# Optimization experiments

Hardware: AMD Instinct MI355X
Metric: run time of the kernel (lower is better)

## Reference

```python
import jax, jax.numpy as jnp
import numpy as np

N_NODES = 50000
N_EDGES = 800000
NFEAT = 512
NHID = 128
NCLASS = 40


def setup_inputs() -> dict:
    key = jax.random.key(0)
    ks = jax.random.split(key, 12)
    s = lambda fan_in: 1.0 / np.sqrt(fan_in)
    return {
        "x": jax.random.normal(ks[0], (N_NODES, NFEAT), dtype=jnp.float32),
        "edge_src": jax.random.randint(ks[1], (N_EDGES,), 0, N_NODES, dtype=jnp.int32),
        "edge_dst": jax.random.randint(ks[2], (N_EDGES,), 0, N_NODES, dtype=jnp.int32),
        "edge_val": jax.random.uniform(ks[3], (N_EDGES,), dtype=jnp.float32) * 0.1,
        # GraphConvolution 1: nfeat -> nhid
        "W1": jax.random.uniform(ks[4], (NFEAT, NHID), jnp.float32, -s(NFEAT), s(NFEAT)),
        "b1": jnp.zeros((NHID,), jnp.float32),
        # res1 Linear: nfeat -> nhid (stored as [in, out])
        "Wr1": jax.random.uniform(ks[5], (NFEAT, NHID), jnp.float32, -s(NFEAT), s(NFEAT)),
        "br1": jnp.zeros((NHID,), jnp.float32),
        # GraphConvolution 2: 2*nhid -> nclass
        "W2": jax.random.uniform(ks[6], (2 * NHID, NCLASS), jnp.float32, -s(2 * NHID), s(2 * NHID)),
        "b2": jnp.zeros((NCLASS,), jnp.float32),
        # res2 Linear: 2*nhid -> nclass
        "Wr2": jax.random.uniform(ks[7], (2 * NHID, NCLASS), jnp.float32, -s(2 * NHID), s(2 * NHID)),
        "br2": jnp.zeros((NCLASS,), jnp.float32),
    }


def _spmm(edge_src, edge_dst, edge_val, support):
    # adj @ support with adj in COO form: out[d] += val * support[s]
    msgs = edge_val[:, None] * support[edge_src]  # [E, F] irregular gather
    return jax.ops.segment_sum(msgs, edge_dst, num_segments=N_NODES)


def reference(x, edge_src, edge_dst, edge_val, W1, b1, Wr1, br1, W2, b2, Wr2, br2):
    # gc1(x, adj) = adj @ (x @ W1) + b1
    gc1 = _spmm(edge_src, edge_dst, edge_val, x @ W1) + b1
    h = jnp.concatenate([jax.nn.relu(gc1), x @ Wr1 + br1], axis=1)  # [N, 2*nhid]
    # dropout is identity in eval mode
    gc2 = _spmm(edge_src, edge_dst, edge_val, h @ W2) + b2
    h2 = gc2 + (h @ Wr2 + br2)
    return jax.nn.log_softmax(h2, axis=1)
```

## Files before the change

### kernel.cpp

```cpp
#include <hip/hip_runtime.h>
#include <stdint.h>

#define N_NODES 50000
#define N_EDGES 800000
#define NFEAT 512
#define NHID 128
#define NCLASS 40
#define NB 196

typedef __attribute__((ext_vector_type(8))) __bf16 bf16x8;
typedef __attribute__((ext_vector_type(4))) float f32x4;

__device__ __forceinline__ uint16_t f2b(float f) {
  uint32_t x = __float_as_uint(f);
  uint32_t r = (x + 0x7fffu + ((x >> 16) & 1u)) >> 16;
  return (uint16_t)r;
}
__device__ __forceinline__ float b2f(uint16_t u) {
  return __uint_as_float(((uint32_t)u) << 16);
}

__global__ void k_prep_w1(const float* __restrict__ W1, const float* __restrict__ Wr1,
                          uint16_t* __restrict__ WT) {
  int idx = blockIdx.x * 256 + threadIdx.x;
  if (idx >= 256 * 512) return;
  int n = idx >> 9, k = idx & 511;
  float v = (n < 128) ? W1[(size_t)k * 128 + n] : Wr1[(size_t)k * 128 + (n - 128)];
  WT[idx] = f2b(v);
}

__global__ void k_prep_w2(const float* __restrict__ W2, const float* __restrict__ Wr2,
                          uint16_t* __restrict__ WT) {
  int idx = blockIdx.x * 256 + threadIdx.x;
  if (idx >= 128 * 256) return;
  int n = idx >> 8, k = idx & 255;
  float v = 0.f;
  if (n < 40) v = W2[(size_t)k * 40 + n];
  else if (n < 80) v = Wr2[(size_t)k * 40 + (n - 40)];
  WT[idx] = f2b(v);
}

__global__ void k_hist(const int* __restrict__ dst, int* __restrict__ counts) {
  int e = blockIdx.x * 256 + threadIdx.x;
  if (e < N_EDGES) atomicAdd(&counts[dst[e]], 1);
}

__global__ void k_blocksum(const int* __restrict__ counts, int* __restrict__ blocksums) {
  __shared__ int red[256];
  int t = threadIdx.x, idx = blockIdx.x * 256 + t;
  red[t] = (idx < N_NODES) ? counts[idx] : 0;
  __syncthreads();
  for (int o = 128; o; o >>= 1) {
    if (t < o) red[t] += red[t + o];
    __syncthreads();
  }
  if (t == 0) blocksums[blockIdx.x] = red[0];
}

__global__ void k_scan2(const int* __restrict__ counts, const int* __restrict__ blocksums,
                        int* __restrict__ offs) {
  __shared__ int red[256];
  __shared__ int sc[256];
  int b = blockIdx.x, t = threadIdx.x;
  red[t] = (t < b && t < NB) ? blocksums[t] : 0;
  __syncthreads();
  for (int o = 128; o; o >>= 1) {
    if (t < o) red[t] += red[t + o];
    __syncthreads();
  }
  int prefix = red[0];
  int idx = b * 256 + t;
  int c = (idx < N_NODES) ? counts[idx] : 0;
  sc[t] = c;
  __syncthreads();
  for (int o = 1; o < 256; o <<= 1) {
    int v = (t >= o) ? sc[t - o] : 0;
    __syncthreads();
    sc[t] += v;
    __syncthreads();
  }
  if (idx <= N_NODES) offs[idx] = prefix + sc[t] - c;
}

__global__ void k_scatter(const int* __restrict__ src, const int* __restrict__ dst,
                          const float* __restrict__ val, const int* __restrict__ offs,
                          int* __restrict__ cursor, int2* __restrict__ es) {
  int e = blockIdx.x * 256 + threadIdx.x;
  if (e >= N_EDGES) return;
  int d = dst[e];
  int pos = offs[d] + atomicAdd(&cursor[d], 1);
  es[pos] = make_int2(src[e], __float_as_int(val[e]));
}

__global__ __launch_bounds__(512) void k_gemm1_fused(
    const float* __restrict__ x, const uint16_t* __restrict__ BT,
    uint16_t* __restrict__ S1b, uint16_t* __restrict__ h, const float* __restrict__ br1) {
  __shared__ uint16_t Al[128 * 72];
  __shared__ uint16_t Bl[256 * 64];
  const int tid = threadIdx.x;
  const int w = tid >> 6, lane = tid & 63;
  const int wm = w >> 2, wn = w & 3;
  const int m0 = blockIdx.x * 128;
  const int M = N_NODES;

  f32x4 acc[4][4];
#pragma unroll
  for (int t = 0; t < 4; t++)
#pragma unroll
    for (int u = 0; u < 4; u++) acc[t][u] = (f32x4)0.f;

  const int arow = tid >> 2;
  const int aslot = tid & 3;
  int ar = m0 + arow;
  if (ar >= M) ar = M - 1;
  const float* gxbase = x + (size_t)ar * NFEAT + aslot * 16;

  for (int kb = 0; kb < 8; ++kb) {
    __syncthreads();
    const int k0 = kb * 64;
    {
      const float4* gp = (const float4*)(gxbase + k0);
      float4 f0 = gp[0], f1 = gp[1], f2 = gp[2], f3 = gp[3];
      union { uint16_t u[8]; uint4 v; } o0, o1;
      o0.u[0] = f2b(f0.x); o0.u[1] = f2b(f0.y); o0.u[2] = f2b(f0.z); o0.u[3] = f2b(f0.w);
      o0.u[4] = f2b(f1.x); o0.u[5] = f2b(f1.y); o0.u[6] = f2b(f1.z); o0.u[7] = f2b(f1.w);
      o1.u[0] = f2b(f2.x); o1.u[1] = f2b(f2.y); o1.u[2] = f2b(f2.z); o1.u[3] = f2b(f2.w);
      o1.u[4] = f2b(f3.x); o1.u[5] = f2b(f3.y); o1.u[6] = f2b(f3.z); o1.u[7] = f2b(f3.w);
      *(uint4*)&Al[arow * 72 + aslot * 16] = o0.v;
      *(uint4*)&Al[arow * 72 + aslot * 16 + 8] = o1.v;
    }
#pragma unroll
    for (int i = 0; i < 4; i++) {
      int chunk = w * 4 + i;
      const uint16_t* gB = BT + (size_t)(chunk * 8 + (lane >> 3)) * NFEAT + k0 + (lane & 7) * 8;
      __builtin_amdgcn_global_load_lds(
          (const __attribute__((address_space(1))) void*)gB,
          (__attribute__((address_space(3))) void*)&Bl[chunk * 512], 16, 0, 0);
    }
    __syncthreads();
#pragma unroll
    for (int s = 0; s < 2; s++) {
      bf16x8 av[4], bv[4];
#pragma unroll
      for (int t = 0; t < 4; t++)
        av[t] = *(const bf16x8*)&Al[(wm * 64 + t * 16 + (lane & 15)) * 72 + s * 32 + (lane >> 4) * 8];
#pragma unroll
      for (int u = 0; u < 4; u++)
        bv[u] = *(const bf16x8*)&Bl[(wn * 64 + u * 16 + (lane & 15)) * 64 + s * 32 + (lane >> 4) * 8];
#pragma unroll
      for (int t = 0; t < 4; t++)
#pragma unroll
        for (int u = 0; u < 4; u++)
          acc[t][u] = __builtin_amdgcn_mfma_f32_16x16x32_bf16(av[t], bv[u], acc[t][u], 0, 0, 0);
    }
  }

  const int cl = lane & 15, rq = lane >> 4;
#pragma unroll
  for (int t = 0; t < 4; t++) {
#pragma unroll
    for (int u = 0; u < 4; u++) {
#pragma unroll
      for (int r = 0; r < 4; r++) {
        int m = m0 + wm * 64 + t * 16 + rq * 4 + r;
        int n = wn * 64 + u * 16 + cl;
        if (m >= M) continue;
        float v = acc[t][u][r];
        if (n < 128)
          S1b[(size_t)m * 128 + n] = f2b(v);
        else
          h[(size_t)m * 256 + n] = f2b(v + br1[n - 128]);
      }
    }
  }
}

__global__ __launch_bounds__(256, 2) void k_gemm2(
    const uint16_t* __restrict__ A, const uint16_t* __restrict__ BT, int M,
    uint16_t* __restrict__ S2b, float* __restrict__ oacc,
    const float* __restrict__ b2, const float* __restrict__ br2) {
  __shared__ uint16_t Al[128 * 64];
  __shared__ uint16_t Bl[128 * 64];
  const int tid = threadIdx.x;
  const int w = tid >> 6, lane = tid & 63;
  const int wm = w >> 1, wn = w & 1;
  const int m0 = blockIdx.x * 128;
  const int K = 256;

  f32x4 acc[4][4];
#pragma unroll
  for (int t = 0; t < 4; t++)
#pragma unroll
    for (int u = 0; u < 4; u++) acc[t][u] = (f32x4)0.f;

  const int lrow = lane >> 3;
  const int lcol = lane & 7;

  for (int kb = 0; kb < K / 64; ++kb) {
    __syncthreads();
    const int k0 = kb * 64;
#pragma unroll
    for (int i = 0; i < 4; i++) {
      int rr = (w * 4 + i) * 8 + lrow;
      int ra = m0 + rr;
      if (ra >= M) ra = M - 1;
      const uint16_t* gA = A + (size_t)ra * K + k0 + lcol * 8;
      __builtin_amdgcn_global_load_lds(
          (const __attribute__((address_space(1))) void*)gA,
          (__attribute__((address_space(3))) void*)&Al[(w * 4 + i) * 512], 16, 0, 0);
      const uint16_t* gB = BT + (size_t)rr * K + k0 + lcol * 8;
      __builtin_amdgcn_global_load_lds(
          (const __attribute__((address_space(1))) void*)gB,
          (__attribute__((address_space(3))) void*)&Bl[(w * 4 + i) * 512], 16, 0, 0);
    }
    __syncthreads();
#pragma unroll
    for (int s = 0; s < 2; s++) {
      bf16x8 av[4], bv[4];
#pragma unroll
      for (int t = 0; t < 4; t++)
        av[t] = *(const bf16x8*)&Al[(wm * 64 + t * 16 + (lane & 15)) * 64 + s * 32 + (lane >> 4) * 8];
#pragma unroll
      for (int u = 0; u < 4; u++)
        bv[u] = *(const bf16x8*)&Bl[(wn * 64 + u * 16 + (lane & 15)) * 64 + s * 32 + (lane >> 4) * 8];
#pragma unroll
      for (int t = 0; t < 4; t++)
#pragma unroll
        for (int u = 0; u < 4; u++)
          acc[t][u] = __builtin_amdgcn_mfma_f32_16x16x32_bf16(av[t], bv[u], acc[t][u], 0, 0, 0);
    }
  }

  const int cl = lane & 15, rq = lane >> 4;
#pragma unroll
  for (int t = 0; t < 4; t++) {
#pragma unroll
    for (int u = 0; u < 4; u++) {
#pragma unroll
      for (int r = 0; r < 4; r++) {
        int m = m0 + wm * 64 + t * 16 + rq * 4 + r;
        int n = wn * 64 + u * 16 + cl;
        if (m >= M) continue;
        float v = acc[t][u][r];
        if (n < 40) S2b[(size_t)m * 64 + n] = f2b(v);
        else if (n < 64) S2b[(size_t)m * 64 + n] = 0;
        if (n >= 40 && n < 80) oacc[(size_t)m * 64 + (n - 40)] = v + b2[n - 40] + br2[n - 40];
        else if (n >= 80 && n < 104) oacc[(size_t)m * 64 + (n - 40)] = 0.f;
      }
    }
  }
}

__global__ void k_spmm1_csr(const int* __restrict__ offs, const int2* __restrict__ es,
                            const uint16_t* __restrict__ S1b, const float* __restrict__ b1,
                            uint16_t* __restrict__ h) {
  int node = blockIdx.x * 4 + (threadIdx.x >> 6);
  if (node >= N_NODES) return;
  int lane = threadIdx.x & 63;
  int eg = lane >> 4;
  int fg = lane & 15;
  int beg = offs[node], end = offs[node + 1];
  float a[8];
#pragma unroll
  for (int j = 0; j < 8; j++) a[j] = 0.f;
  for (int p = beg; p < end; p += 4) {
    int pe = p + eg;
    bool ok = pe < end;
    int2 ev = es[ok ? pe : beg];
    float v = ok ? __int_as_float(ev.y) : 0.f;
    uint4 g = *(const uint4*)(S1b + (size_t)ev.x * 128 + fg * 8);
    a[0] += v * b2f((uint16_t)g.x); a[1] += v * b2f((uint16_t)(g.x >> 16));
    a[2] += v * b2f((uint16_t)g.y); a[3] += v * b2f((uint16_t)(g.y >> 16));
    a[4] += v * b2f((uint16_t)g.z); a[5] += v * b2f((uint16_t)(g.z >> 16));
    a[6] += v * b2f((uint16_t)g.w); a[7] += v * b2f((uint16_t)(g.w >> 16));
  }
#pragma unroll
  for (int j = 0; j < 8; j++) {
    a[j] += __shfl_xor(a[j], 16, 64);
    a[j] += __shfl_xor(a[j], 32, 64);
  }
  if (eg == 0) {
    const float4* bp = (const float4*)(b1 + fg * 8);
    float4 ba = bp[0], bb = bp[1];
    float r0 = a[0] + ba.x, r1 = a[1] + ba.y, r2 = a[2] + ba.z, r3 = a[3] + ba.w;
    float r4 = a[4] + bb.x, r5 = a[5] + bb.y, r6 = a[6] + bb.z, r7 = a[7] + bb.w;
    union { uint16_t u[8]; uint4 v; } o;
    o.u[0] = f2b(r0 > 0.f ? r0 : 0.f); o.u[1] = f2b(r1 > 0.f ? r1 : 0.f);
    o.u[2] = f2b(r2 > 0.f ? r2 : 0.f); o.u[3] = f2b(r3 > 0.f ? r3 : 0.f);
    o.u[4] = f2b(r4 > 0.f ? r4 : 0.f); o.u[5] = f2b(r5 > 0.f ? r5 : 0.f);
    o.u[6] = f2b(r6 > 0.f ? r6 : 0.f); o.u[7] = f2b(r7 > 0.f ? r7 : 0.f);
    *(uint4*)(h + (size_t)node * 256 + fg * 8) = o.v;
  }
}

__global__ void k_spmm2_lsm(const int* __restrict__ offs, const int2* __restrict__ es,
                            const uint16_t* __restrict__ S2b, const float* __restrict__ oacc,
                            float* __restrict__ out) {
  int node = blockIdx.x * 4 + (threadIdx.x >> 6);
  if (node >= N_NODES) return;
  int lane = threadIdx.x & 63;
  int eg = lane >> 3;
  int fg = lane & 7;
  int beg = offs[node], end = offs[node + 1];
  float a[8];
#pragma unroll
  for (int j = 0; j < 8; j++) a[j] = 0.f;
  for (int p = beg; p < end; p += 8) {
    int pe = p + eg;
    bool ok = pe < end;
    int2 ev = es[ok ? pe : beg];
    float v = ok ? __int_as_float(ev.y) : 0.f;
    uint4 g = *(const uint4*)(S2b + (size_t)ev.x * 64 + fg * 8);
    a[0] += v * b2f((uint16_t)g.x); a[1] += v * b2f((uint16_t)(g.x >> 16));
    a[2] += v * b2f((uint16_t)g.y); a[3] += v * b2f((uint16_t)(g.y >> 16));
    a[4] += v * b2f((uint16_t)g.z); a[5] += v * b2f((uint16_t)(g.z >> 16));
    a[6] += v * b2f((uint16_t)g.w); a[7] += v * b2f((uint16_t)(g.w >> 16));
  }
#pragma unroll
  for (int j = 0; j < 8; j++) {
    a[j] += __shfl_xor(a[j], 8, 64);
    a[j] += __shfl_xor(a[j], 16, 64);
    a[j] += __shfl_xor(a[j], 32, 64);
  }
  const float4* op = (const float4*)(oacc + (size_t)node * 64 + fg * 8);
  float4 o0 = op[0], o1 = op[1];
  float v0 = a[0] + o0.x, v1 = a[1] + o0.y, v2 = a[2] + o0.z, v3 = a[3] + o0.w;
  float v4 = a[4] + o1.x, v5 = a[5] + o1.y, v6 = a[6] + o1.z, v7 = a[7] + o1.w;
  bool valid = fg < 5;
  float m01 = v0 > v1 ? v0 : v1, m23 = v2 > v3 ? v2 : v3;
  float m45 = v4 > v5 ? v4 : v5, m67 = v6 > v7 ? v6 : v7;
  float ml = m01 > m23 ? m01 : m23;
  float mh = m45 > m67 ? m45 : m67;
  float mv = ml > mh ? ml : mh;
  mv = valid ? mv : -1e30f;
#pragma unroll
  for (int o = 1; o <= 4; o <<= 1) {
    float t = __shfl_xor(mv, o, 64);
    mv = mv > t ? mv : t;
  }
  float se = 0.f;
  if (valid)
    se = __expf(v0 - mv) + __expf(v1 - mv) + __expf(v2 - mv) + __expf(v3 - mv) +
         __expf(v4 - mv) + __expf(v5 - mv) + __expf(v6 - mv) + __expf(v7 - mv);
#pragma unroll
  for (int o = 1; o <= 4; o <<= 1) se += __shfl_xor(se, o, 64);
  if (eg == 0 && valid) {
    float ls = mv + __logf(se);
    float4 r0 = make_float4(v0 - ls, v1 - ls, v2 - ls, v3 - ls);
    float4 r1 = make_float4(v4 - ls, v5 - ls, v6 - ls, v7 - ls);
    float4* wp = (float4*)(out + (size_t)node * 40 + fg * 8);
    wp[0] = r0;
    wp[1] = r1;
  }
}

extern "C" void kernel_launch(void* const* d_in, const int* in_sizes, int n_in,
                              void* d_out, int out_size, void* d_ws, size_t ws_size,
                              hipStream_t stream) {
  const float* x = (const float*)d_in[0];
  const int* esrc = (const int*)d_in[1];
  const int* edst = (const int*)d_in[2];
  const float* eval = (const float*)d_in[3];
  const float* W1 = (const float*)d_in[4];
  const float* b1 = (const float*)d_in[5];
  const float* Wr1 = (const float*)d_in[6];
  const float* br1 = (const float*)d_in[7];
  const float* W2 = (const float*)d_in[8];
  const float* b2 = (const float*)d_in[9];
  const float* Wr2 = (const float*)d_in[10];
  const float* br2 = (const float*)d_in[11];
  float* out = (float*)d_out;

  char* ws = (char*)d_ws;
  uint16_t* S1b  = (uint16_t*)(ws);
  uint16_t* h    = (uint16_t*)(ws + 12800000);
  uint16_t* WT1  = (uint16_t*)(ws + 38400000);
  uint16_t* WT2  = (uint16_t*)(ws + 38662144);
  uint16_t* S2b  = (uint16_t*)(ws + 38727680);
  float*    oacc = (float*)(ws + 45127680);
  int*      counts = (int*)(ws + 57927680);
  int*      cursor = (int*)(ws + 58127680);
  int*      offs   = (int*)(ws + 58327680);
  int2*     es     = (int2*)(ws + 58527744);
  int*      blocksums = (int*)(ws + 64927744);

  hipMemsetAsync(counts, 0, 400000, stream);

  k_prep_w1<<<(256 * 512) / 256, 256, 0, stream>>>(W1, Wr1, WT1);
  k_prep_w2<<<(128 * 256) / 256, 256, 0, stream>>>(W2, Wr2, WT2);

  k_hist<<<(N_EDGES + 255) / 256, 256, 0, stream>>>(edst, counts);
  k_blocksum<<<NB, 256, 0, stream>>>(counts, blocksums);
  k_scan2<<<NB, 256, 0, stream>>>(counts, blocksums, offs);
  k_scatter<<<(N_EDGES + 255) / 256, 256, 0, stream>>>(esrc, edst, eval, offs, cursor, es);

  k_gemm1_fused<<<391, 512, 0, stream>>>(x, WT1, S1b, h, br1);

  k_spmm1_csr<<<(N_NODES + 3) / 4, 256, 0, stream>>>(offs, es, S1b, b1, h);

  k_gemm2<<<391, 256, 0, stream>>>(h, WT2, N_NODES, S2b, oacc, b2, br2);

  k_spmm2_lsm<<<(N_NODES + 3) / 4, 256, 0, stream>>>(offs, es, S2b, oacc, out);
}
```

Measured before the change: 364.7 us.

## Split x bf16 cast into separate kernel and tile GEMM1 over N

Adds a standalone kernel that casts x to bf16 in workspace, then rewrites GEMM1 to load both A and B tiles into LDS with direct global-to-LDS loads. GEMM1 now uses 256-thread blocks over a 2D grid (128x128 tiles) instead of 512-thread blocks covering all 256 output columns. The intent is to remove the in-loop fp32 load and convert work and raise occupancy. In exchange it adds an extra 100 MB of global read plus a 51 MB write for the bf16 copy, and x is read once per N tile.

```diff
diff --git a/kernel.cpp b/kernel.cpp
--- a/kernel.cpp
+++ b/kernel.cpp
@@ -18,6 +18,17 @@
 }
 __device__ __forceinline__ float b2f(uint16_t u) {
   return __uint_as_float(((uint32_t)u) << 16);
+}
+
+__global__ void k_cast_x(const float* __restrict__ x, uint16_t* __restrict__ xb, int n8) {
+  int i = blockIdx.x * blockDim.x + threadIdx.x;
+  if (i >= n8) return;
+  const float4* p = (const float4*)x + (size_t)i * 2;
+  float4 a = p[0], b = p[1];
+  union { uint16_t u[8]; uint4 v; } o;
+  o.u[0] = f2b(a.x); o.u[1] = f2b(a.y); o.u[2] = f2b(a.z); o.u[3] = f2b(a.w);
+  o.u[4] = f2b(b.x); o.u[5] = f2b(b.y); o.u[6] = f2b(b.z); o.u[7] = f2b(b.w);
+  ((uint4*)xb)[i] = o.v;
 }
 
 __global__ void k_prep_w1(const float* __restrict__ W1, const float* __restrict__ Wr1,
@@ -92,16 +103,17 @@
   es[pos] = make_int2(src[e], __float_as_int(val[e]));
 }
 
-__global__ __launch_bounds__(512) void k_gemm1_fused(
-    const float* __restrict__ x, const uint16_t* __restrict__ BT,
+__global__ __launch_bounds__(256, 2) void k_gemm1(
+    const uint16_t* __restrict__ A, const uint16_t* __restrict__ BT, int M,
     uint16_t* __restrict__ S1b, uint16_t* __restrict__ h, const float* __restrict__ br1) {
-  __shared__ uint16_t Al[128 * 72];
-  __shared__ uint16_t Bl[256 * 64];
+  __shared__ uint16_t Al[128 * 64];
+  __shared__ uint16_t Bl[128 * 64];
   const int tid = threadIdx.x;
   const int w = tid >> 6, lane = tid & 63;
-  const int wm = w >> 2, wn = w & 3;
+  const int wm = w >> 1, wn = w & 1;
   const int m0 = blockIdx.x * 128;
-  const int M = N_NODES;
+  const int n0 = blockIdx.y * 128;
+  const int K = NFEAT;
 
   f32x4 acc[4][4];
 #pragma unroll
@@ -109,33 +121,26 @@
 #pragma unroll
     for (int u = 0; u < 4; u++) acc[t][u] = (f32x4)0.f;
 
-  const int arow = tid >> 2;
-  const int aslot = tid & 3;
-  int ar = m0 + arow;
-  if (ar >= M) ar = M - 1;
-  const float* gxbase = x + (size_t)ar * NFEAT + aslot * 16;
-
-  for (int kb = 0; kb < 8; ++kb) {
+  const int lrow = lane >> 3;
+  const int lcol = lane & 7;
+
+  for (int kb = 0; kb < K / 64; ++kb) {
     __syncthreads();
     const int k0 = kb * 64;
-    {
-      const float4* gp = (const float4*)(gxbase + k0);
-      float4 f0 = gp[0], f1 = gp[1], f2 = gp[2], f3 = gp[3];
-      union { uint16_t u[8]; uint4 v; } o0, o1;
-      o0.u[0] = f2b(f0.x); o0.u[1] = f2b(f0.y); o0.u[2] = f2b(f0.z); o0.u[3] = f2b(f0.w);
-      o0.u[4] = f2b(f1.x); o0.u[5] = f2b(f1.y); o0.u[6] = f2b(f1.z); o0.u[7] = f2b(f1.w);
-      o1.u[0] = f2b(f2.x); o1.u[1] = f2b(f2.y); o1.u[2] = f2b(f2.z); o1.u[3] = f2b(f2.w);
-      o1.u[4] = f2b(f3.x); o1.u[5] = f2b(f3.y); o1.u[6] = f2b(f3.z); o1.u[7] = f2b(f3.w);
-      *(uint4*)&Al[arow * 72 + aslot * 16] = o0.v;
-      *(uint4*)&Al[arow * 72 + aslot * 16 + 8] = o1.v;
-    }
 #pragma unroll
     for (int i = 0; i < 4; i++) {
-      int chunk = w * 4 + i;
-      const uint16_t* gB = BT + (size_t)(chunk * 8 + (lane >> 3)) * NFEAT + k0 + (lane & 7) * 8;
+      int rr = (w * 4 + i) * 8 + lrow;
+      int ra = m0 + rr;
+      if (ra >= M) ra = M - 1;
+      const uint16_t* gA = A + (size_t)ra * K + k0 + lcol * 8;
+      __builtin_amdgcn_global_load_lds(
+          (const __attribute__((address_space(1))) void*)gA,
+          (__attribute__((address_space(3))) void*)&Al[(w * 4 + i) * 512], 16, 0, 0);
+      int rb = n0 + rr;
+      const uint16_t* gB = BT + (size_t)rb * K + k0 + lcol * 8;
       __builtin_amdgcn_global_load_lds(
           (const __attribute__((address_space(1))) void*)gB,
-          (__attribute__((address_space(3))) void*)&Bl[chunk * 512], 16, 0, 0);
+          (__attribute__((address_space(3))) void*)&Bl[(w * 4 + i) * 512], 16, 0, 0);
     }
     __syncthreads();
 #pragma unroll
@@ -143,7 +148,7 @@
       bf16x8 av[4], bv[4];
 #pragma unroll
       for (int t = 0; t < 4; t++)
-        av[t] = *(const bf16x8*)&Al[(wm * 64 + t * 16 + (lane & 15)) * 72 + s * 32 + (lane >> 4) * 8];
+        av[t] = *(const bf16x8*)&Al[(wm * 64 + t * 16 + (lane & 15)) * 64 + s * 32 + (lane >> 4) * 8];
 #pragma unroll
       for (int u = 0; u < 4; u++)
         bv[u] = *(const bf16x8*)&Bl[(wn * 64 + u * 16 + (lane & 15)) * 64 + s * 32 + (lane >> 4) * 8];
@@ -163,7 +168,7 @@
 #pragma unroll
       for (int r = 0; r < 4; r++) {
         int m = m0 + wm * 64 + t * 16 + rq * 4 + r;
-        int n = wn * 64 + u * 16 + cl;
+        int n = n0 + wn * 64 + u * 16 + cl;
         if (m >= M) continue;
         float v = acc[t][u][r];
         if (n < 128)
@@ -372,20 +377,22 @@
   float* out = (float*)d_out;
 
   char* ws = (char*)d_ws;
-  uint16_t* S1b  = (uint16_t*)(ws);
-  uint16_t* h    = (uint16_t*)(ws + 12800000);
-  uint16_t* WT1  = (uint16_t*)(ws + 38400000);
-  uint16_t* WT2  = (uint16_t*)(ws + 38662144);
-  uint16_t* S2b  = (uint16_t*)(ws + 38727680);
-  float*    oacc = (float*)(ws + 45127680);
-  int*      counts = (int*)(ws + 57927680);
-  int*      cursor = (int*)(ws + 58127680);
-  int*      offs   = (int*)(ws + 58327680);
-  int2*     es     = (int2*)(ws + 58527744);
-  int*      blocksums = (int*)(ws + 64927744);
+  uint16_t* xb   = (uint16_t*)(ws);
+  uint16_t* S1b  = (uint16_t*)(ws + 51200000);
+  uint16_t* h    = (uint16_t*)(ws + 64000000);
+  uint16_t* WT1  = (uint16_t*)(ws + 89600000);
+  uint16_t* WT2  = (uint16_t*)(ws + 89862144);
+  uint16_t* S2b  = (uint16_t*)(ws + 89927680);
+  float*    oacc = (float*)(ws + 96327680);
+  int*      counts = (int*)(ws + 109127680);
+  int*      cursor = (int*)(ws + 109327680);
+  int*      offs   = (int*)(ws + 109527680);
+  int2*     es     = (int2*)(ws + 109727696);
+  int*      blocksums = (int*)(ws + 116127696);
 
   hipMemsetAsync(counts, 0, 400000, stream);
 
+  k_cast_x<<<(3200000 + 255) / 256, 256, 0, stream>>>(x, xb, 3200000);
   k_prep_w1<<<(256 * 512) / 256, 256, 0, stream>>>(W1, Wr1, WT1);
   k_prep_w2<<<(128 * 256) / 256, 256, 0, stream>>>(W2, Wr2, WT2);
 
@@ -394,7 +401,8 @@
   k_scan2<<<NB, 256, 0, stream>>>(counts, blocksums, offs);
   k_scatter<<<(N_EDGES + 255) / 256, 256, 0, stream>>>(esrc, edst, eval, offs, cursor, es);
 
-  k_gemm1_fused<<<391, 512, 0, stream>>>(x, WT1, S1b, h, br1);
+  dim3 g1(391, 2);
+  k_gemm1<<<g1, 256, 0, stream>>>(xb, WT1, N_NODES, S1b, h, br1);
 
   k_spmm1_csr<<<(N_NODES + 3) / 4, 256, 0, stream>>>(offs, es, S1b, b1, h);
 
```

Result: slower. 382.5 us (+4.9%).
